# Kernel tuning notes

Hardware: AMD Instinct MI355X
Metric: run time of the kernel (lower is better)

Reference implementation:

```python
import jax, jax.numpy as jnp
import numpy as np

LEN = 20_000_000  # samples per channel (interleaved real/imag), divisible by 10


def setup_inputs() -> dict:
    key = jax.random.key(0)
    k0, k1, k2, k3 = jax.random.split(key, 4)
    in0 = jax.random.normal(k0, (LEN,), dtype=jnp.float32)
    in1 = jax.random.normal(k1, (LEN,), dtype=jnp.float32)
    in2 = jax.random.normal(k2, (LEN,), dtype=jnp.float32)
    in3 = jax.random.normal(k3, (LEN,), dtype=jnp.float32)
    # bf buffer: ones with imaginary parts (odd indices) zeroed
    bf = jnp.ones((1, 8), dtype=jnp.float32).at[0, 1::2].set(0.0)
    return {"in0": in0, "in1": in1, "in2": in2, "in3": in3, "bf": bf}


def reference(in0, in1, in2, in3, bf):
    # Deinterleave real/imag, stack channels -> (4, N), reshape to (B, 4, 5)
    in_real = jnp.stack((in0[::2], in1[::2], in2[::2], in3[::2]), axis=0).reshape(-1, 4, 5)
    in_imag = jnp.stack((in0[1::2], in1[1::2], in2[1::2], in3[1::2]), axis=0).reshape(-1, 4, 5)
    bf_real = bf[0, ::2].reshape(1, 1, 4)
    bf_imag = bf[0, 1::2].reshape(1, 1, 4)
    # Complex matmul: (1,1,4) @ (B,4,5) -> (B,1,5)
    out_real = jnp.matmul(bf_real, in_real) - jnp.matmul(bf_imag, in_imag)
    out_imag = jnp.matmul(bf_imag, in_real) + jnp.matmul(bf_real, in_imag)
    result = jnp.concatenate([out_real, out_imag], axis=2)  # (B,1,10)
    # Faithful to original: strided scatter on dim 1 (size 1) -> no-op copy
    result2 = jnp.zeros_like(result)
    result2 = result2.at[:, ::2].set(result[:, :5])
    result2 = result2.at[:, 1::2].set(result[:, 5:])
    return result2
```

## Files before the change

### kernel.cpp

```cpp
#include <hip/hip_runtime.h>
#include <hip/hip_bf16.h>


__global__ __launch_bounds__(256) void beamform_kernel(
    const float* __restrict__ in0, const float* __restrict__ in1,
    const float* __restrict__ in2, const float* __restrict__ in3,
    const float* __restrict__ bf, float* __restrict__ out,
    int blocksPerChannel, int threadsPerChannel)
{
    const int tid = blockIdx.x * blockDim.x + threadIdx.x;
    if (tid >= threadsPerChannel) return;
    const int ch = blockIdx.y;

    const float* __restrict__ in =
        (ch == 0) ? in0 : (ch == 1) ? in1 : (ch == 2) ? in2 : in3;

    const int bl = tid / 5;
    const int c  = tid - bl * 5;

    const float2* __restrict__ p =
        reinterpret_cast<const float2*>(in + (size_t)bl * 40 + 2 * c);
    const float2 x0 = p[0];
    const float2 x1 = p[5];
    const float2 x2 = p[10];
    const float2 x3 = p[15];

    const float br0 = bf[0], bi0 = bf[1];
    const float br1 = bf[2], bi1 = bf[3];
    const float br2 = bf[4], bi2 = bf[5];
    const float br3 = bf[6], bi3 = bf[7];

    float re = br0 * x0.x - bi0 * x0.y;
    float im = bi0 * x0.x + br0 * x0.y;
    re += br1 * x1.x - bi1 * x1.y;
    im += bi1 * x1.x + br1 * x1.y;
    re += br2 * x2.x - bi2 * x2.y;
    im += bi2 * x2.x + br2 * x2.y;
    re += br3 * x3.x - bi3 * x3.y;
    im += bi3 * x3.x + br3 * x3.y;

    const size_t b = (size_t)ch * blocksPerChannel + bl;
    float* __restrict__ o = out + b * 10;
    o[c] = re;
    o[5 + c] = im;
}

extern "C" void kernel_launch(void* const* d_in, const int* in_sizes, int n_in,
                              void* d_out, int out_size, void* d_ws, size_t ws_size,
                              hipStream_t stream)
{
    const float* in0 = (const float*)d_in[0];
    const float* in1 = (const float*)d_in[1];
    const float* in2 = (const float*)d_in[2];
    const float* in3 = (const float*)d_in[3];
    const float* bf  = (const float*)d_in[4];
    float* out = (float*)d_out;

    const int len = in_sizes[0];
    const int blocksPerChannel = len / 40;
    const int threadsPerChannel = blocksPerChannel * 5;

    const int block = 256;
    dim3 grid((threadsPerChannel + block - 1) / block, 4, 1);
    beamform_kernel<<<grid, dim3(block, 1, 1), 0, stream>>>(
        in0, in1, in2, in3, bf, out, blocksPerChannel, threadsPerChannel);
}
```

Baseline: 287.0 us.

## Stage input and output through LDS for coalesced float4/float2 global access

Each workgroup now handles 256 beamforming blocks: it loads the contiguous input tile with fully coalesced float4 reads into shared memory, computes from LDS, and writes results back through an LDS buffer as coalesced float2 stores. This replaces the strided float2 loads and scattered scalar stores of the per-thread version. It costs about 50KB of LDS per workgroup, which limits occupancy, and adds two barriers per workgroup.

```diff
diff --git a/kernel.cpp b/kernel.cpp
--- a/kernel.cpp
+++ b/kernel.cpp
@@ -2,47 +2,94 @@
 #include <hip/hip_bf16.h>
 
 
-__global__ __launch_bounds__(256) void beamform_kernel(
+#define BLOCKS_PER_WG 256
+#define WG 256
+
+__global__ __launch_bounds__(WG) void beamform_kernel(
     const float* __restrict__ in0, const float* __restrict__ in1,
     const float* __restrict__ in2, const float* __restrict__ in3,
     const float* __restrict__ bf, float* __restrict__ out,
-    int blocksPerChannel, int threadsPerChannel)
+    int blocksPerChannel)
 {
-    const int tid = blockIdx.x * blockDim.x + threadIdx.x;
-    if (tid >= threadsPerChannel) return;
+    __shared__ __align__(16) float lds_in[BLOCKS_PER_WG * 40];
+    __shared__ __align__(16) float lds_out[BLOCKS_PER_WG * 10];
+
+    const int t = threadIdx.x;
+    const int g = blockIdx.x;
     const int ch = blockIdx.y;
 
     const float* __restrict__ in =
         (ch == 0) ? in0 : (ch == 1) ? in1 : (ch == 2) ? in2 : in3;
 
-    const int bl = tid / 5;
-    const int c  = tid - bl * 5;
-
-    const float2* __restrict__ p =
-        reinterpret_cast<const float2*>(in + (size_t)bl * 40 + 2 * c);
-    const float2 x0 = p[0];
-    const float2 x1 = p[5];
-    const float2 x2 = p[10];
-    const float2 x3 = p[15];
+    const int blockStart = g * BLOCKS_PER_WG;
+    const int nblk = min(BLOCKS_PER_WG, blocksPerChannel - blockStart);
 
     const float br0 = bf[0], bi0 = bf[1];
     const float br1 = bf[2], bi1 = bf[3];
     const float br2 = bf[4], bi2 = bf[5];
     const float br3 = bf[6], bi3 = bf[7];
 
-    float re = br0 * x0.x - bi0 * x0.y;
-    float im = bi0 * x0.x + br0 * x0.y;
-    re += br1 * x1.x - bi1 * x1.y;
-    im += bi1 * x1.x + br1 * x1.y;
-    re += br2 * x2.x - bi2 * x2.y;
-    im += bi2 * x2.x + br2 * x2.y;
-    re += br3 * x3.x - bi3 * x3.y;
-    im += bi3 * x3.x + br3 * x3.y;
+    const float4* __restrict__ gin =
+        reinterpret_cast<const float4*>(in + (size_t)blockStart * 40);
 
-    const size_t b = (size_t)ch * blocksPerChannel + bl;
-    float* __restrict__ o = out + b * 10;
-    o[c] = re;
-    o[5 + c] = im;
+    if (nblk == BLOCKS_PER_WG) {
+#pragma unroll
+        for (int k = 0; k < 10; ++k) {
+            const int f = k * WG + t;
+            float4 v = gin[f];
+            *reinterpret_cast<float4*>(&lds_in[4 * f]) = v;
+        }
+    } else {
+        const int nf4 = nblk * 10;
+#pragma unroll
+        for (int k = 0; k < 10; ++k) {
+            const int f = k * WG + t;
+            if (f < nf4) {
+                float4 v = gin[f];
+                *reinterpret_cast<float4*>(&lds_in[4 * f]) = v;
+            }
+        }
+    }
+    __syncthreads();
+
+#pragma unroll
+    for (int k = 0; k < 5; ++k) {
+        const int tt = k * WG + t;
+        if (tt < nblk * 5) {
+            const int bl = tt / 5;
+            const int c  = tt - bl * 5;
+            const float* __restrict__ x = &lds_in[40 * bl + 2 * c];
+            const float2 x0 = *reinterpret_cast<const float2*>(&x[0]);
+            const float2 x1 = *reinterpret_cast<const float2*>(&x[10]);
+            const float2 x2 = *reinterpret_cast<const float2*>(&x[20]);
+            const float2 x3 = *reinterpret_cast<const float2*>(&x[30]);
+
+            float re = br0 * x0.x - bi0 * x0.y;
+            float im = bi0 * x0.x + br0 * x0.y;
+            re += br1 * x1.x - bi1 * x1.y;
+            im += bi1 * x1.x + br1 * x1.y;
+            re += br2 * x2.x - bi2 * x2.y;
+            im += bi2 * x2.x + br2 * x2.y;
+            re += br3 * x3.x - bi3 * x3.y;
+            im += bi3 * x3.x + br3 * x3.y;
+
+            lds_out[10 * bl + c]     = re;
+            lds_out[10 * bl + 5 + c] = im;
+        }
+    }
+    __syncthreads();
+
+    const float2* __restrict__ lo = reinterpret_cast<const float2*>(lds_out);
+    float2* __restrict__ gout = reinterpret_cast<float2*>(
+        out + ((size_t)ch * blocksPerChannel + blockStart) * 10);
+    const int nf2 = nblk * 5;
+#pragma unroll
+    for (int k = 0; k < 5; ++k) {
+        const int j = k * WG + t;
+        if (j < nf2) {
+            gout[j] = lo[j];
+        }
+    }
 }
 
 extern "C" void kernel_launch(void* const* d_in, const int* in_sizes, int n_in,
@@ -58,10 +105,8 @@
 
     const int len = in_sizes[0];
     const int blocksPerChannel = len / 40;
-    const int threadsPerChannel = blocksPerChannel * 5;
 
-    const int block = 256;
-    dim3 grid((threadsPerChannel + block - 1) / block, 4, 1);
-    beamform_kernel<<<grid, dim3(block, 1, 1), 0, stream>>>(
-        in0, in1, in2, in3, bf, out, blocksPerChannel, threadsPerChannel);
+    dim3 grid((blocksPerChannel + BLOCKS_PER_WG - 1) / BLOCKS_PER_WG, 4, 1);
+    beamform_kernel<<<grid, dim3(WG, 1, 1), 0, stream>>>(
+        in0, in1, in2, in3, bf, out, blocksPerChannel);
 }
```

After: 297.9 us. 3.8% more time.
